# Optimization experiments

Hardware: AMD Instinct MI355X
Metric: run time of the kernel (lower is better)

## Reference

```python
import jax, jax.numpy as jnp
import numpy as np

F = 64
N_HIT, N_SP, N_OPH, N_PMT, N_OPF, N_EVT = 300_000, 50_000, 200_000, 30_000, 2_000, 256


def setup_inputs() -> dict:
    key = jax.random.key(0)
    ks = iter(jax.random.split(key, 64))

    def feats(n):
        return jax.random.normal(next(ks), (n, F), jnp.float32)

    def edges(n_src, n_dst, e):
        s = jax.random.randint(next(ks), (e,), 0, n_src)
        d = jax.random.randint(next(ks), (e,), 0, n_dst)
        return jnp.stack([s, d]).astype(jnp.int32)

    def p(shape, scale=0.05):
        return jax.random.normal(next(ks), shape, jnp.float32) * scale

    return {
        "x_hit": feats(N_HIT), "x_sp": feats(N_SP), "x_oph": feats(N_OPH),
        "x_pmt": feats(N_PMT), "x_opf": feats(N_OPF), "x_evt": feats(N_EVT),
        # 10 NuGraphBlocks, all with source=target=out=F (planes=1), stacked on dim 0
        "edge_w": p((10, 2 * F, 1)), "edge_b": p((10, 1)),
        "w1": p((10, 2 * F, F)), "b1": p((10, F)),
        "w2": p((10, F, F)), "b2": p((10, F)),
        "e_hit_sp": edges(N_HIT, N_SP, 300_000),
        "e_oph_pmt": edges(N_OPH, N_PMT, 400_000),
        "e_pmt_opf": edges(N_PMT, N_OPF, 60_000),
        "e_sp_evt": edges(N_SP, N_EVT, 50_000),
        "e_opf_evt": edges(N_OPF, N_EVT, 2_000),
        "e_evt_sp": edges(N_EVT, N_SP, 50_000),
        "e_sp_hit": edges(N_SP, N_HIT, 300_000),
        "e_evt_opf": edges(N_EVT, N_OPF, 2_000),
        "e_opf_pmt": edges(N_OPF, N_PMT, 60_000),
        "e_pmt_oph": edges(N_PMT, N_OPH, 400_000),
    }


def _mish(x):
    return x * jnp.tanh(jax.nn.softplus(x))


def _block(i, x_src, x_tgt, e, edge_w, edge_b, w1, b1, w2, b2):
    """NuGraphBlock: sigmoid edge attention + softmax aggregation + Mish MLP."""
    s, d = e[0], e[1]
    x_j = x_src[s]            # [E, F] source features on edges
    x_i = x_tgt[d]            # [E, F] target features on edges
    cat = jax.lax.stop_gradient(jnp.concatenate([x_i, x_j], axis=1))  # .detach()
    w = jax.nn.sigmoid(cat @ edge_w[i] + edge_b[i])   # [E, 1]
    m = w * x_j                                       # messages [E, F]
    n_tgt = x_tgt.shape[0]
    # PyG SoftmaxAggregation (t=1): featurewise softmax over each target segment
    mx = jax.ops.segment_max(m, d, num_segments=n_tgt)
    ex = jnp.exp(m - mx[d])
    den = jax.ops.segment_sum(ex, d, num_segments=n_tgt)
    alpha = ex / (den[d] + 1e-16)
    aggr = jax.ops.segment_sum(alpha * m, d, num_segments=n_tgt)  # [n_tgt, F]
    h = jnp.concatenate([aggr, x_tgt], axis=1)
    h = _mish(h @ w1[i] + b1[i])
    return _mish(h @ w2[i] + b2[i])


def reference(x_hit, x_sp, x_oph, x_pmt, x_opf, x_evt,
              edge_w, edge_b, w1, b1, w2, b2,
              e_hit_sp, e_oph_pmt, e_pmt_opf, e_sp_evt, e_opf_evt,
              e_evt_sp, e_sp_hit, e_evt_opf, e_opf_pmt, e_pmt_oph):
    P = (edge_w, edge_b, w1, b1, w2, b2)
    n = _block(0, x_hit, x_sp, e_hit_sp, *P)                         # plane_to_nexus
    pmt = _block(1, x_oph, x_pmt, e_oph_pmt, *P)                     # hit_to_pmt
    opf = _block(2, pmt, x_opf, e_pmt_opf, *P)                       # pmt_to_flash
    i = (_block(3, n, x_evt, e_sp_evt, *P)
         + _block(4, opf, x_evt, e_opf_evt, *P))                     # nexus_flash_to_interaction (HeteroConv sum)
    n = _block(5, i, n, e_evt_sp, *P)                                # interaction_to_nexus
    p = _block(6, n, x_hit, e_sp_hit, *P)                            # nexus_to_plane
    opf = _block(7, i, opf, e_evt_opf, *P)                           # interaction_to_flash
    pmt = _block(8, opf, pmt, e_opf_pmt, *P)                         # flash_to_pmt
    oph = _block(9, pmt, x_oph, e_pmt_oph, *P)                       # pmt_to_ophit
    return (p, n, oph, pmt, opf, i)
```

## Files before the change

kernel.cpp:

```cpp
#include <hip/hip_runtime.h>
#include <hip/hip_bf16.h>


typedef __bf16 bf16x8 __attribute__((ext_vector_type(8)));
typedef float  f32x4  __attribute__((ext_vector_type(4)));

__device__ __forceinline__ float b2f(ushort u) {
    return (float)__builtin_bit_cast(__bf16, u);
}
__device__ __forceinline__ ushort f2b(float f) {
    __bf16 h = (__bf16)f;
    return __builtin_bit_cast(ushort, h);
}
__device__ __forceinline__ __bf16 bhi(float x) { return (__bf16)x; }
__device__ __forceinline__ __bf16 blo(float x) {
    __bf16 h = (__bf16)x;
    return (__bf16)(x - (float)h);
}

__device__ __forceinline__ float ldx(const void* p, long i, int isb) {
    return isb ? b2f(((const ushort*)p)[i]) : ((const float*)p)[i];
}
__device__ __forceinline__ f32x4 ldx4(const void* p, long i, int isb) {
    f32x4 r;
    if (isb) {
        uint2 v = *(const uint2*)((const ushort*)p + i);
        r[0] = b2f((ushort)(v.x & 0xffff));
        r[1] = b2f((ushort)(v.x >> 16));
        r[2] = b2f((ushort)(v.y & 0xffff));
        r[3] = b2f((ushort)(v.y >> 16));
    } else {
        r = *(const f32x4*)((const float*)p + i);
    }
    return r;
}

__device__ __forceinline__ float frcp(float x) {
    return __builtin_amdgcn_rcpf(x);
}

__device__ __forceinline__ float mishf(float x) {
    float t = __expf(x);
    float u = 1.0f + t;
    float r = 1.0f - 2.0f * frcp(u * u + 1.0f);
    return x * r;
}

__global__ __launch_bounds__(256) void detect_kernel(const ushort* __restrict__ u,
                                                     int* __restrict__ flag)
{
    __shared__ int s_cnt;
    if (threadIdx.x == 0) s_cnt = 0;
    __syncthreads();
    int cnt = 0;
    for (int i = threadIdx.x; i < 8192; i += 256) {
        ushort v = u[2 * i];
        if ((v & 0x7F80u) == 0x7F80u) cnt++;
    }
#pragma unroll
    for (int off = 32; off; off >>= 1) cnt += __shfl_xor(cnt, off, 64);
    if ((threadIdx.x & 63) == 0) atomicAdd(&s_cnt, cnt);
    __syncthreads();
    if (threadIdx.x == 0) flag[0] = (s_cnt == 0) ? 1 : 0;
}

__global__ __launch_bounds__(256) void edge_kernel(
    const void* xsrc, long sOff, int smode,
    const void* xtgt, long tOff, int tmode,
    const int* __restrict__ eidx, int E,
    const void* ew, long ewOff, const void* eb, long ebOff,
    float* __restrict__ den, float* __restrict__ num,
    int lo, int hi, const int* __restrict__ flagp)
{
    int isb = flagp[0];
    int sm = (smode == 2) ? isb : smode;
    int tm = (tmode == 2) ? isb : tmode;

    int lane = threadIdx.x & 63;
    float wI = ldx(ew, ewOff + lane, isb);
    float wJ = ldx(ew, ewOff + 64 + lane, isb);
    float bias = ldx(eb, ebOff, isb);

    int nwaves = gridDim.x * 4;
    for (int e = blockIdx.x * 4 + (threadIdx.x >> 6); e < E; e += nwaves) {
        int d = eidx[E + e];
        if (d < lo || d >= hi) continue;
        int s = eidx[e];

        float xj = ldx(xsrc, sOff + (long)s * 64 + lane, sm);
        float xi = ldx(xtgt, tOff + (long)d * 64 + lane, tm);
        float part = xi * wI + xj * wJ;
#pragma unroll
        for (int off = 32; off; off >>= 1) part += __shfl_xor(part, off, 64);
        float t = part + bias;
        float w = frcp(1.0f + __expf(-t));
        float m = w * xj;
        float ex = __expf(m);
        long idx = (long)(d - lo) * 64 + lane;
        unsafeAtomicAdd(&den[idx], ex);
        unsafeAtomicAdd(&num[idx], ex * m);
    }
}

__global__ __launch_bounds__(256) void mlp_kernel(
    const float* __restrict__ den, const float* __restrict__ num,
    const void* xt, long xtOff, int tmode,
    const void* w1, long w1Off, const void* b1, long b1Off,
    const void* w2, long w2Off, const void* b2, long b2Off,
    float* outf, void* outd, long outOff,
    int lo, int hi, int accumulate, const int* __restrict__ flagp)
{
    __shared__ __align__(16) ushort W1t[64][144];
    __shared__ __align__(16) ushort W2t[64][80];
    __shared__ __align__(16) float  A2s[4][16][68];

    int isb = flagp[0];
    int tm = (tmode == 2) ? isb : tmode;
    ushort* ob16 = nullptr;
    float*  ob32 = nullptr;
    if (outd) {
        if (isb) ob16 = (ushort*)outd + outOff;
        else     ob32 = (float*)outd + outOff;
    }

    for (int idx = threadIdx.x; idx < 128 * 64; idx += 256) {
        int k = idx >> 6, n = idx & 63;
        W1t[n][k] = f2b(ldx(w1, w1Off + idx, isb));
    }
    for (int idx = threadIdx.x; idx < 64 * 64; idx += 256) {
        int k = idx >> 6, n = idx & 63;
        W2t[n][k] = f2b(ldx(w2, w2Off + idx, isb));
    }
    __syncthreads();

    int wid = threadIdx.x >> 6, lane = threadIdx.x & 63;
    int m16 = lane & 15, quad = lane >> 4;
    int ntiles = (hi - lo + 15) >> 4;

    for (int tile = blockIdx.x * 4 + wid; tile < ntiles; tile += gridDim.x * 4) {
        int base = lo + (tile << 4);
        int nodeA = base + m16;
        if (nodeA > hi - 1) nodeA = hi - 1;
        long aggoff = (long)(nodeA - lo) * 64;
        long xoff   = (long)nodeA * 64;

        bf16x8 Ahi[4], Alo[4];
#pragma unroll
        for (int s2 = 0; s2 < 2; ++s2) {
            int k0 = s2 * 32 + quad * 8;
            f32x4 n0v = *(const f32x4*)(num + aggoff + k0);
            f32x4 n1v = *(const f32x4*)(num + aggoff + k0 + 4);
            f32x4 d0v = *(const f32x4*)(den + aggoff + k0);
            f32x4 d1v = *(const f32x4*)(den + aggoff + k0 + 4);
#pragma unroll
            for (int j = 0; j < 4; ++j) {
                float a0 = n0v[j] * frcp(d0v[j] + 1e-16f);
                float a1 = n1v[j] * frcp(d1v[j] + 1e-16f);
                Ahi[s2][j]     = bhi(a0);
                Alo[s2][j]     = blo(a0);
                Ahi[s2][j + 4] = bhi(a1);
                Alo[s2][j + 4] = blo(a1);
            }
        }
#pragma unroll
        for (int s2 = 2; s2 < 4; ++s2) {
            int k0 = (s2 - 2) * 32 + quad * 8;
            f32x4 x0 = ldx4(xt, xtOff + xoff + k0, tm);
            f32x4 x1 = ldx4(xt, xtOff + xoff + k0 + 4, tm);
#pragma unroll
            for (int j = 0; j < 4; ++j) {
                Ahi[s2][j]     = bhi(x0[j]);
                Alo[s2][j]     = blo(x0[j]);
                Ahi[s2][j + 4] = bhi(x1[j]);
                Alo[s2][j + 4] = blo(x1[j]);
            }
        }

        f32x4 acc[4] = {};
#pragma unroll
        for (int t = 0; t < 4; ++t) {
#pragma unroll
            for (int s = 0; s < 4; ++s) {
                bf16x8 B = __builtin_bit_cast(bf16x8,
                    *(const int4*)&W1t[t * 16 + m16][s * 32 + quad * 8]);
                acc[t] = __builtin_amdgcn_mfma_f32_16x16x32_bf16(Ahi[s], B, acc[t], 0, 0, 0);
                acc[t] = __builtin_amdgcn_mfma_f32_16x16x32_bf16(Alo[s], B, acc[t], 0, 0, 0);
            }
        }
#pragma unroll
        for (int t = 0; t < 4; ++t) {
            float bias = ldx(b1, b1Off + t * 16 + m16, isb);
#pragma unroll
            for (int r = 0; r < 4; ++r) {
                float x = acc[t][r] + bias;
                A2s[wid][quad * 4 + r][t * 16 + m16] = mishf(x);
            }
        }
        asm volatile("s_waitcnt lgkmcnt(0)" ::: "memory");

        bf16x8 A2hi[2], A2lo[2];
#pragma unroll
        for (int s2 = 0; s2 < 2; ++s2) {
            int k0 = s2 * 32 + quad * 8;
            f32x4 h0 = *(const f32x4*)&A2s[wid][m16][k0];
            f32x4 h1 = *(const f32x4*)&A2s[wid][m16][k0 + 4];
#pragma unroll
            for (int j = 0; j < 4; ++j) {
                A2hi[s2][j]     = bhi(h0[j]);
                A2lo[s2][j]     = blo(h0[j]);
                A2hi[s2][j + 4] = bhi(h1[j]);
                A2lo[s2][j + 4] = blo(h1[j]);
            }
        }
        f32x4 acc2[4] = {};
#pragma unroll
        for (int t = 0; t < 4; ++t) {
#pragma unroll
            for (int s = 0; s < 2; ++s) {
                bf16x8 B = __builtin_bit_cast(bf16x8,
                    *(const int4*)&W2t[t * 16 + m16][s * 32 + quad * 8]);
                acc2[t] = __builtin_amdgcn_mfma_f32_16x16x32_bf16(A2hi[s], B, acc2[t], 0, 0, 0);
                acc2[t] = __builtin_amdgcn_mfma_f32_16x16x32_bf16(A2lo[s], B, acc2[t], 0, 0, 0);
            }
        }
#pragma unroll
        for (int t = 0; t < 4; ++t) {
            float bias = ldx(b2, b2Off + t * 16 + m16, isb);
#pragma unroll
            for (int r = 0; r < 4; ++r) {
                int node = base + quad * 4 + r;
                if (node < hi) {
                    long idx = (long)node * 64 + t * 16 + m16;
                    float y = mishf(acc2[t][r] + bias);
                    if (accumulate)
                        y += outf ? outf[idx] : (ob16 ? b2f(ob16[idx]) : ob32[idx]);
                    if (outf) outf[idx] = y;
                    if (ob16) ob16[idx] = f2b(y);
                    else if (ob32) ob32[idx] = y;
                }
            }
        }
    }
}

struct HBuf { const void* base; long off; int mode; };

static void run_block(HBuf src, HBuf tgt, const int* e, int E, int n_tgt, int bi,
                      const void* edge_w, const void* edge_b,
                      const void* w1, const void* b1,
                      const void* w2, const void* b2,
                      float* den, float* num, int chunkCap,
                      float* outf, void* outd, long outOff, int accumulate,
                      const int* flagp, hipStream_t stream)
{
    for (int lo = 0; lo < n_tgt; lo += chunkCap) {
        int hi = lo + chunkCap < n_tgt ? lo + chunkCap : n_tgt;
        size_t bytes = (size_t)(hi - lo) * 64 * 4;
        if (hi - lo == chunkCap) {
            (void)hipMemsetAsync(den, 0, 2 * bytes, stream);
        } else {
            (void)hipMemsetAsync(den, 0, bytes, stream);
            (void)hipMemsetAsync(num, 0, bytes, stream);
        }
        int eblocks = (E + 3) / 4;
        if (eblocks > 2048) eblocks = 2048;
        edge_kernel<<<eblocks, 256, 0, stream>>>(
            src.base, src.off, src.mode, tgt.base, tgt.off, tgt.mode,
            e, E, edge_w, (long)bi * 128, edge_b, (long)bi,
            den, num, lo, hi, flagp);
        int ntiles = (hi - lo + 15) / 16;
        int mblocks = (ntiles + 3) / 4;
        if (mblocks > 2048) mblocks = 2048;
        mlp_kernel<<<mblocks, 256, 0, stream>>>(
            den, num, tgt.base, tgt.off, tgt.mode,
            w1, (long)bi * 128 * 64, b1, (long)bi * 64,
            w2, (long)bi * 64 * 64, b2, (long)bi * 64,
            outf, outd, outOff, lo, hi, accumulate, flagp);
    }
}

extern "C" void kernel_launch(void* const* d_in, const int* in_sizes, int n_in,
                              void* d_out, int out_size, void* d_ws, size_t ws_size,
                              hipStream_t stream)
{
    (void)in_sizes; (void)n_in; (void)out_size;

    const void* x_hit = d_in[0];
    const void* x_sp  = d_in[1];
    const void* x_oph = d_in[2];
    const void* x_pmt = d_in[3];
    const void* x_opf = d_in[4];
    const void* x_evt = d_in[5];
    const void* edge_w = d_in[6];
    const void* edge_b = d_in[7];
    const void* w1 = d_in[8];
    const void* b1 = d_in[9];
    const void* w2 = d_in[10];
    const void* b2 = d_in[11];
    const int* e_hit_sp  = (const int*)d_in[12];
    const int* e_oph_pmt = (const int*)d_in[13];
    const int* e_pmt_opf = (const int*)d_in[14];
    const int* e_sp_evt  = (const int*)d_in[15];
    const int* e_opf_evt = (const int*)d_in[16];
    const int* e_evt_sp  = (const int*)d_in[17];
    const int* e_sp_hit  = (const int*)d_in[18];
    const int* e_evt_opf = (const int*)d_in[19];
    const int* e_opf_pmt = (const int*)d_in[20];
    const int* e_pmt_oph = (const int*)d_in[21];

    const long off_p = 0, off_n = 19200000, off_oph = 22400000,
               off_pmt = 35200000, off_opf = 37120000, off_i = 37248000;

    char* wsc = (char*)d_ws;
    int* flagp = (int*)(wsc + ((ws_size - 64) & ~(size_t)15));
    size_t usable = ws_size > 256 ? ws_size - 256 : 0;
    float* wsf = (float*)d_ws;

    detect_kernel<<<1, 256, 0, stream>>>((const ushort*)x_hit, flagp);

    const size_t nodeFloats = 3200000ull * 2 + 1920000ull * 2 + 128000ull * 2 + 16384ull;
    const size_t nodeBytes  = nodeFloats * 4;
    bool fp32path = usable >= nodeBytes + (8ull << 20);
    size_t capBytes = fp32path ? (usable - nodeBytes) : usable;
    long cap = (long)(capBytes / 512);
    if (cap > 300000) cap = 300000;
    cap &= ~15L;
    if (cap < 16) cap = 16;
    int chunkCap = (int)cap;

    float* den = fp32path ? (wsf + nodeFloats) : wsf;
    float* num = den + (size_t)chunkCap * 64;

    HBuf bhit{x_hit, 0, 2}, bsp{x_sp, 0, 2}, boph{x_oph, 0, 2},
         bpmt{x_pmt, 0, 2}, bopf{x_opf, 0, 2}, bevt{x_evt, 0, 2};

#define W edge_w, edge_b, w1, b1, w2, b2, den, num, chunkCap
    if (fp32path) {
        float* n0   = wsf;
        float* n1   = n0 + 3200000;
        float* pmt0 = n1 + 3200000;
        float* pmt1 = pmt0 + 1920000;
        float* opf0 = pmt1 + 1920000;
        float* opf1 = opf0 + 128000;
        float* iA   = opf1 + 128000;
        HBuf bn0{n0, 0, 0}, bn1{n1, 0, 0}, bpmt0{pmt0, 0, 0}, bpmt1{pmt1, 0, 0},
             bopf0{opf0, 0, 0}, bopf1{opf1, 0, 0}, biA{iA, 0, 0};

        run_block(bhit,  bsp,   e_hit_sp,  300000,  50000, 0, W, n0,   nullptr, 0,      0, flagp, stream);
        run_block(boph,  bpmt,  e_oph_pmt, 400000,  30000, 1, W, pmt0, nullptr, 0,      0, flagp, stream);
        run_block(bpmt0, bopf,  e_pmt_opf,  60000,   2000, 2, W, opf0, nullptr, 0,      0, flagp, stream);
        run_block(bn0,   bevt,  e_sp_evt,   50000,    256, 3, W, iA,   d_out, off_i,    0, flagp, stream);
        run_block(bopf0, bevt,  e_opf_evt,   2000,    256, 4, W, iA,   d_out, off_i,    1, flagp, stream);
        run_block(biA,   bn0,   e_evt_sp,   50000,  50000, 5, W, n1,   d_out, off_n,    0, flagp, stream);
        run_block(bn1,   bhit,  e_sp_hit,  300000, 300000, 6, W, nullptr, d_out, off_p, 0, flagp, stream);
        run_block(biA,   bopf0, e_evt_opf,   2000,   2000, 7, W, opf1, d_out, off_opf,  0, flagp, stream);
        run_block(bopf1, bpmt0, e_opf_pmt,  60000,  30000, 8, W, pmt1, d_out, off_pmt,  0, flagp, stream);
        run_block(bpmt1, boph,  e_pmt_oph, 400000, 200000, 9, W, nullptr, d_out, off_oph, 0, flagp, stream);
    } else {
        HBuf dn{d_out, off_n, 2}, dpmt{d_out, off_pmt, 2}, dopf{d_out, off_opf, 2},
             di{d_out, off_i, 2};

        run_block(bhit, bsp,  e_hit_sp,  300000,  50000, 0, W, nullptr, d_out, off_n,   0, flagp, stream);
        run_block(boph, bpmt, e_oph_pmt, 400000,  30000, 1, W, nullptr, d_out, off_pmt, 0, flagp, stream);
        run_block(dpmt, bopf, e_pmt_opf,  60000,   2000, 2, W, nullptr, d_out, off_opf, 0, flagp, stream);
        run_block(dn,   bevt, e_sp_evt,   50000,    256, 3, W, nullptr, d_out, off_i,   0, flagp, stream);
        run_block(dopf, bevt, e_opf_evt,   2000,    256, 4, W, nullptr, d_out, off_i,   1, flagp, stream);
        run_block(di,   dn,   e_evt_sp,   50000,  50000, 5, W, nullptr, d_out, off_n,   0, flagp, stream);
        run_block(dn,   bhit, e_sp_hit,  300000, 300000, 6, W, nullptr, d_out, off_p,   0, flagp, stream);
        run_block(di,   dopf, e_evt_opf,   2000,   2000, 7, W, nullptr, d_out, off_opf, 0, flagp, stream);
        run_block(dopf, dpmt, e_opf_pmt,  60000,  30000, 8, W, nullptr, d_out, off_pmt, 0, flagp, stream);
        run_block(dpmt, boph, e_pmt_oph, 400000, 200000, 9, W, nullptr, d_out, off_oph, 0, flagp, stream);
    }
#undef W
}
```

Baseline: 1.533 ms.

## Bucket-sort edges by target tile and aggregate softmax in shared memory

```diff
diff --git a/kernel.cpp b/kernel.cpp
--- a/kernel.cpp
+++ b/kernel.cpp
@@ -46,6 +46,41 @@
     return x * r;
 }
 
+#define NLIST 10
+#define E0 300000
+#define E1 400000
+#define E2 60000
+#define E3 50000
+#define E4 2000
+#define E5 50000
+#define E6 300000
+#define E7 2000
+#define E8 60000
+#define E9 400000
+#define ETOT 1624000
+#define SH0 5
+#define SH1 4
+#define SH2 0
+#define SH3 0
+#define SH4 0
+#define SH5 5
+#define SH6 6
+#define SH7 0
+#define SH8 4
+#define SH9 6
+#define GB0 0
+#define GB1 1563
+#define GB2 3438
+#define GB3 5438
+#define GB4 5694
+#define GB5 5950
+#define GB6 7513
+#define GB7 12201
+#define GB8 14201
+#define GB9 16076
+#define NB_TOTAL 19201
+#define NB_PAD   19456
+
 __global__ __launch_bounds__(256) void detect_kernel(const ushort* __restrict__ u,
                                                      int* __restrict__ flag)
 {
@@ -64,6 +99,130 @@
     if (threadIdx.x == 0) flag[0] = (s_cnt == 0) ? 1 : 0;
 }
 
+__global__ __launch_bounds__(256) void count_kernel(
+    const int* __restrict__ e0, const int* __restrict__ e1,
+    const int* __restrict__ e2, const int* __restrict__ e3,
+    const int* __restrict__ e4, const int* __restrict__ e5,
+    const int* __restrict__ e6, const int* __restrict__ e7,
+    const int* __restrict__ e8, const int* __restrict__ e9,
+    int* __restrict__ cnt)
+{
+    long gid = (long)blockIdx.x * 256 + threadIdx.x;
+    long gstride = (long)gridDim.x * 256;
+#define CSEG(EP, EN, GB, SHV) \
+    for (long i = gid; i < (EN); i += gstride) { \
+        int d = (EP)[(EN) + i]; \
+        atomicAdd(&cnt[(GB) + (d >> (SHV))], 1); \
+    }
+    CSEG(e0, E0, GB0, SH0) CSEG(e1, E1, GB1, SH1) CSEG(e2, E2, GB2, SH2)
+    CSEG(e3, E3, GB3, SH3) CSEG(e4, E4, GB4, SH4) CSEG(e5, E5, GB5, SH5)
+    CSEG(e6, E6, GB6, SH6) CSEG(e7, E7, GB7, SH7) CSEG(e8, E8, GB8, SH8)
+    CSEG(e9, E9, GB9, SH9)
+#undef CSEG
+}
+
+__global__ __launch_bounds__(256) void scan_kernel(const int* __restrict__ cnt,
+                                                   int* __restrict__ off)
+{
+    __shared__ int wsum[4];
+    int tid = threadIdx.x;
+    const int STRIP = (NB_TOTAL + 255) / 256;
+    int s0 = tid * STRIP;
+    int s1 = s0 + STRIP; if (s1 > NB_TOTAL) s1 = NB_TOTAL;
+    int sum = 0;
+    for (int i = s0; i < s1; ++i) sum += cnt[i];
+    int lane = tid & 63, wid = tid >> 6;
+    int incl = sum;
+#pragma unroll
+    for (int o = 1; o < 64; o <<= 1) {
+        int v = __shfl_up(incl, o, 64);
+        if (lane >= o) incl += v;
+    }
+    if (lane == 63) wsum[wid] = incl;
+    __syncthreads();
+    int wbase = 0;
+    for (int wq = 0; wq < wid; ++wq) wbase += wsum[wq];
+    int run = wbase + incl - sum;
+    for (int i = s0; i < s1; ++i) { off[i] = run; run += cnt[i]; }
+}
+
+__global__ __launch_bounds__(256) void scatter_kernel(
+    const int* __restrict__ e0, const int* __restrict__ e1,
+    const int* __restrict__ e2, const int* __restrict__ e3,
+    const int* __restrict__ e4, const int* __restrict__ e5,
+    const int* __restrict__ e6, const int* __restrict__ e7,
+    const int* __restrict__ e8, const int* __restrict__ e9,
+    int* __restrict__ off, int2* __restrict__ sdv)
+{
+    long gid = (long)blockIdx.x * 256 + threadIdx.x;
+    long gstride = (long)gridDim.x * 256;
+#define SSEG(EP, EN, GB, SHV) \
+    for (long i = gid; i < (EN); i += gstride) { \
+        int s = (EP)[i], d = (EP)[(EN) + i]; \
+        int pos = atomicAdd(&off[(GB) + (d >> (SHV))], 1); \
+        sdv[pos] = make_int2(s, d); \
+    }
+    SSEG(e0, E0, GB0, SH0) SSEG(e1, E1, GB1, SH1) SSEG(e2, E2, GB2, SH2)
+    SSEG(e3, E3, GB3, SH3) SSEG(e4, E4, GB4, SH4) SSEG(e5, E5, GB5, SH5)
+    SSEG(e6, E6, GB6, SH6) SSEG(e7, E7, GB7, SH7) SSEG(e8, E8, GB8, SH8)
+    SSEG(e9, E9, GB9, SH9)
+#undef SSEG
+}
+
+__global__ __launch_bounds__(256) void edge_bucket_kernel(
+    const void* xsrc, long sOff, int smode,
+    const void* xtgt, long tOff, int tmode,
+    const int2* __restrict__ sdv, const int* __restrict__ boff,
+    int gb0, int W, int lo, int hi,
+    const void* ew, long ewOff, const void* eb, long ebOff,
+    float* __restrict__ den, float* __restrict__ num,
+    const int* __restrict__ flagp)
+{
+    __shared__ float acc[64 * 128];
+
+    int isb = flagp[0];
+    int sm = (smode == 2) ? isb : smode;
+    int tm = (tmode == 2) ? isb : tmode;
+
+    int tid = threadIdx.x, lane = tid & 63, wid = tid >> 6;
+    int t0 = lo + blockIdx.x * W;
+    int rows = hi - t0; if (rows > W) rows = W;
+    int gb = gb0 + blockIdx.x;
+    int start = (gb == 0) ? 0 : boff[gb - 1];
+    int end = boff[gb];
+
+    for (int i = tid; i < rows * 128; i += 256) acc[i] = 0.0f;
+    __syncthreads();
+
+    float wI = ldx(ew, ewOff + lane, isb);
+    float wJ = ldx(ew, ewOff + 64 + lane, isb);
+    float bias = ldx(eb, ebOff, isb);
+
+    for (int i = start + wid; i < end; i += 4) {
+        int2 e = sdv[i];
+        float xj = ldx(xsrc, sOff + (long)e.x * 64 + lane, sm);
+        float xi = ldx(xtgt, tOff + (long)e.y * 64 + lane, tm);
+        float part = xi * wI + xj * wJ;
+#pragma unroll
+        for (int o = 32; o; o >>= 1) part += __shfl_xor(part, o, 64);
+        float t = part + bias;
+        float w = frcp(1.0f + __expf(-t));
+        float m = w * xj;
+        float ex = __expf(m);
+        int r = e.y - t0;
+        atomicAdd(&acc[r * 128 + lane], ex);
+        atomicAdd(&acc[r * 128 + 64 + lane], ex * m);
+    }
+    __syncthreads();
+
+    for (int i = tid; i < rows * 16; i += 256) {
+        int r = i >> 4, c = (i & 15) * 4;
+        long go = (long)(t0 - lo + r) * 64 + c;
+        *(f32x4*)&den[go] = *(const f32x4*)&acc[r * 128 + c];
+        *(f32x4*)&num[go] = *(const f32x4*)&acc[r * 128 + 64 + c];
+    }
+}
+
 __global__ __launch_bounds__(256) void edge_kernel(
     const void* xsrc, long sOff, int smode,
     const void* xtgt, long tOff, int tmode,
@@ -86,7 +245,6 @@
         int d = eidx[E + e];
         if (d < lo || d >= hi) continue;
         int s = eidx[e];
-
         float xj = ldx(xsrc, sOff + (long)s * 64 + lane, sm);
         float xi = ldx(xtgt, tOff + (long)d * 64 + lane, tm);
         float part = xi * wI + xj * wJ;
@@ -244,6 +402,36 @@
 }
 
 struct HBuf { const void* base; long off; int mode; };
+
+static void run_block_sorted(HBuf src, HBuf tgt, int n_tgt, int bi,
+                             int gbase, int shift,
+                             const int2* sdv, const int* boff,
+                             const void* edge_w, const void* edge_b,
+                             const void* w1, const void* b1,
+                             const void* w2, const void* b2,
+                             float* den, float* num, int chunkCap,
+                             float* outf, void* outd, long outOff, int accumulate,
+                             const int* flagp, hipStream_t stream)
+{
+    int W = 1 << shift;
+    for (int lo = 0; lo < n_tgt; lo += chunkCap) {
+        int hi = lo + chunkCap < n_tgt ? lo + chunkCap : n_tgt;
+        int nb = (hi - lo + W - 1) >> shift;
+        edge_bucket_kernel<<<nb, 256, 0, stream>>>(
+            src.base, src.off, src.mode, tgt.base, tgt.off, tgt.mode,
+            sdv, boff, gbase + (lo >> shift), W, lo, hi,
+            edge_w, (long)bi * 128, edge_b, (long)bi,
+            den, num, flagp);
+        int ntiles = (hi - lo + 15) / 16;
+        int mblocks = (ntiles + 3) / 4;
+        if (mblocks > 2048) mblocks = 2048;
+        mlp_kernel<<<mblocks, 256, 0, stream>>>(
+            den, num, tgt.base, tgt.off, tgt.mode,
+            w1, (long)bi * 128 * 64, b1, (long)bi * 64,
+            w2, (long)bi * 64 * 64, b2, (long)bi * 64,
+            outf, outd, outOff, lo, hi, accumulate, flagp);
+    }
+}
 
 static void run_block(HBuf src, HBuf tgt, const int* e, int E, int n_tgt, int bi,
                       const void* edge_w, const void* edge_b,
@@ -320,22 +508,70 @@
 
     const size_t nodeFloats = 3200000ull * 2 + 1920000ull * 2 + 128000ull * 2 + 16384ull;
     const size_t nodeBytes  = nodeFloats * 4;
-    bool fp32path = usable >= nodeBytes + (8ull << 20);
-    size_t capBytes = fp32path ? (usable - nodeBytes) : usable;
-    long cap = (long)(capBytes / 512);
-    if (cap > 300000) cap = 300000;
-    cap &= ~15L;
-    if (cap < 16) cap = 16;
-    int chunkCap = (int)cap;
-
-    float* den = fp32path ? (wsf + nodeFloats) : wsf;
-    float* num = den + (size_t)chunkCap * 64;
+    const size_t sortFloats = (size_t)ETOT * 2 + 2 * NB_PAD;
+    const size_t sortBytes  = sortFloats * 4;
+
+    bool sortedPath = usable >= nodeBytes + sortBytes + (4ull << 20);
+    bool fp32path   = usable >= nodeBytes + (8ull << 20);
 
     HBuf bhit{x_hit, 0, 2}, bsp{x_sp, 0, 2}, boph{x_oph, 0, 2},
          bpmt{x_pmt, 0, 2}, bopf{x_opf, 0, 2}, bevt{x_evt, 0, 2};
 
-#define W edge_w, edge_b, w1, b1, w2, b2, den, num, chunkCap
-    if (fp32path) {
+    if (sortedPath) {
+        float* n0   = wsf;
+        float* n1   = n0 + 3200000;
+        float* pmt0 = n1 + 3200000;
+        float* pmt1 = pmt0 + 1920000;
+        float* opf0 = pmt1 + 1920000;
+        float* opf1 = opf0 + 128000;
+        float* iA   = opf1 + 128000;
+        int2* sdv   = (int2*)(wsf + nodeFloats);
+        int* cnt    = (int*)(sdv + ETOT);
+        int* boff   = cnt + NB_PAD;
+        float* den  = (float*)(boff + NB_PAD);
+
+        size_t capBytes = usable - nodeBytes - sortBytes;
+        long cap = (long)(capBytes / 512);
+        if (cap > 300000) cap = 300000;
+        cap &= ~63L;
+        if (cap < 64) cap = 64;
+        int chunkCap = (int)cap;
+        float* num = den + (size_t)chunkCap * 64;
+
+        (void)hipMemsetAsync(cnt, 0, NB_PAD * sizeof(int), stream);
+        count_kernel<<<512, 256, 0, stream>>>(
+            e_hit_sp, e_oph_pmt, e_pmt_opf, e_sp_evt, e_opf_evt,
+            e_evt_sp, e_sp_hit, e_evt_opf, e_opf_pmt, e_pmt_oph, cnt);
+        scan_kernel<<<1, 256, 0, stream>>>(cnt, boff);
+        scatter_kernel<<<512, 256, 0, stream>>>(
+            e_hit_sp, e_oph_pmt, e_pmt_opf, e_sp_evt, e_opf_evt,
+            e_evt_sp, e_sp_hit, e_evt_opf, e_opf_pmt, e_pmt_oph, boff, sdv);
+
+        HBuf bn0{n0, 0, 0}, bn1{n1, 0, 0}, bpmt0{pmt0, 0, 0}, bpmt1{pmt1, 0, 0},
+             bopf0{opf0, 0, 0}, bopf1{opf1, 0, 0}, biA{iA, 0, 0};
+
+#define WS edge_w, edge_b, w1, b1, w2, b2, den, num, chunkCap
+        run_block_sorted(bhit,  bsp,    50000, 0, GB0, SH0, sdv, boff, WS, n0,   nullptr, 0,      0, flagp, stream);
+        run_block_sorted(boph,  bpmt,   30000, 1, GB1, SH1, sdv, boff, WS, pmt0, nullptr, 0,      0, flagp, stream);
+        run_block_sorted(bpmt0, bopf,    2000, 2, GB2, SH2, sdv, boff, WS, opf0, nullptr, 0,      0, flagp, stream);
+        run_block_sorted(bn0,   bevt,     256, 3, GB3, SH3, sdv, boff, WS, iA,   d_out, off_i,    0, flagp, stream);
+        run_block_sorted(bopf0, bevt,     256, 4, GB4, SH4, sdv, boff, WS, iA,   d_out, off_i,    1, flagp, stream);
+        run_block_sorted(biA,   bn0,    50000, 5, GB5, SH5, sdv, boff, WS, n1,   d_out, off_n,    0, flagp, stream);
+        run_block_sorted(bn1,   bhit,  300000, 6, GB6, SH6, sdv, boff, WS, nullptr, d_out, off_p, 0, flagp, stream);
+        run_block_sorted(biA,   bopf0,   2000, 7, GB7, SH7, sdv, boff, WS, opf1, d_out, off_opf,  0, flagp, stream);
+        run_block_sorted(bopf1, bpmt0,  30000, 8, GB8, SH8, sdv, boff, WS, pmt1, d_out, off_pmt,  0, flagp, stream);
+        run_block_sorted(bpmt1, boph,  200000, 9, GB9, SH9, sdv, boff, WS, nullptr, d_out, off_oph, 0, flagp, stream);
+#undef WS
+    } else if (fp32path) {
+        size_t capBytes = usable - nodeBytes;
+        long cap = (long)(capBytes / 512);
+        if (cap > 300000) cap = 300000;
+        cap &= ~15L;
+        if (cap < 16) cap = 16;
+        int chunkCap = (int)cap;
+        float* den = wsf + nodeFloats;
+        float* num = den + (size_t)chunkCap * 64;
+
         float* n0   = wsf;
         float* n1   = n0 + 3200000;
         float* pmt0 = n1 + 3200000;
@@ -346,6 +582,7 @@
         HBuf bn0{n0, 0, 0}, bn1{n1, 0, 0}, bpmt0{pmt0, 0, 0}, bpmt1{pmt1, 0, 0},
              bopf0{opf0, 0, 0}, bopf1{opf1, 0, 0}, biA{iA, 0, 0};
 
+#define W edge_w, edge_b, w1, b1, w2, b2, den, num, chunkCap
         run_block(bhit,  bsp,   e_hit_sp,  300000,  50000, 0, W, n0,   nullptr, 0,      0, flagp, stream);
         run_block(boph,  bpmt,  e_oph_pmt, 400000,  30000, 1, W, pmt0, nullptr, 0,      0, flagp, stream);
         run_block(bpmt0, bopf,  e_pmt_opf,  60000,   2000, 2, W, opf0, nullptr, 0,      0, flagp, stream);
@@ -356,10 +593,19 @@
         run_block(biA,   bopf0, e_evt_opf,   2000,   2000, 7, W, opf1, d_out, off_opf,  0, flagp, stream);
         run_block(bopf1, bpmt0, e_opf_pmt,  60000,  30000, 8, W, pmt1, d_out, off_pmt,  0, flagp, stream);
         run_block(bpmt1, boph,  e_pmt_oph, 400000, 200000, 9, W, nullptr, d_out, off_oph, 0, flagp, stream);
+#undef W
     } else {
+        long cap = (long)(usable / 512);
+        if (cap > 300000) cap = 300000;
+        cap &= ~15L;
+        if (cap < 16) cap = 16;
+        int chunkCap = (int)cap;
+        float* den = wsf;
+        float* num = den + (size_t)chunkCap * 64;
+
         HBuf dn{d_out, off_n, 2}, dpmt{d_out, off_pmt, 2}, dopf{d_out, off_opf, 2},
              di{d_out, off_i, 2};
-
+#define W edge_w, edge_b, w1, b1, w2, b2, den, num, chunkCap
         run_block(bhit, bsp,  e_hit_sp,  300000,  50000, 0, W, nullptr, d_out, off_n,   0, flagp, stream);
         run_block(boph, bpmt, e_oph_pmt, 400000,  30000, 1, W, nullptr, d_out, off_pmt, 0, flagp, stream);
         run_block(dpmt, bopf, e_pmt_opf,  60000,   2000, 2, W, nullptr, d_out, off_opf, 0, flagp, stream);
@@ -370,6 +616,6 @@
         run_block(di,   dopf, e_evt_opf,   2000,   2000, 7, W, nullptr, d_out, off_opf, 0, flagp, stream);
         run_block(dopf, dpmt, e_opf_pmt,  60000,  30000, 8, W, nullptr, d_out, off_pmt, 0, flagp, stream);
         run_block(dpmt, boph, e_pmt_oph, 400000, 200000, 9, W, nullptr, d_out, off_oph, 0, flagp, stream);
-    }
 #undef W
-}
+    }
+}
```

After: 2.446 ms. 59.6% more time.
